# Kernel optimization log

Hardware: AMD Instinct MI355X
Metric: run time of the kernel (lower is better)

## Reference

```python
import jax, jax.numpy as jnp
import numpy as np

B, T, IN, H = 4096, 128, 768, 256


def setup_inputs() -> dict:
    key = jax.random.key(0)
    ks = jax.random.split(key, 5)
    s1 = 1.0 / np.sqrt(IN)
    s2 = 1.0 / np.sqrt(H)
    return {
        "x": jax.random.normal(ks[0], (B, IN), jnp.float32),
        "W1": jax.random.normal(ks[1], (T, IN, H), jnp.float32) * s1,
        "b1": jnp.zeros((T, H), jnp.float32),
        "W2": jax.random.normal(ks[2], (T, H, H), jnp.float32) * s2,
        "b2": jnp.zeros((T, H), jnp.float32),
        "W3": jax.random.normal(ks[3], (T, H), jnp.float32) * s2,
        "b3": jnp.zeros((T,), jnp.float32),
    }


def reference(x, W1, b1, W2, b2, W3, b3):
    # Per-task 3-layer MLP, vectorized over tasks. Dropout is eval-mode (identity).
    h = jax.nn.relu(jnp.einsum('bi,tih->bth', x, W1) + b1)          # [B, T, H]
    h = jax.nn.relu(jnp.einsum('bth,thk->btk', h, W2) + b2)         # [B, T, H]
    out = jnp.einsum('bth,th->bt', h, W3) + b3                      # [B, T]
    return out
```

## Files before the change

### kernel.cpp

```cpp
#include <hip/hip_runtime.h>
#include <cstdint>
#include <cstddef>

#define B_   4096
#define T_   128
#define IN_  768
#define H_   256
#define BM_  128
#define KC1  (IN_ / 32)
#define KC2  (H_ / 32)

typedef __bf16 bf16_t;
typedef bf16_t bf16x8  __attribute__((ext_vector_type(8)));
typedef bf16_t bf16x4  __attribute__((ext_vector_type(4)));
typedef float  floatx16 __attribute__((ext_vector_type(16)));

#define MFMA32(a, b, c) __builtin_amdgcn_mfma_f32_32x32x16_bf16((a), (b), (c), 0, 0, 0)

__device__ __forceinline__ void gl_lds16(const bf16_t* g, bf16_t* l) {
    __builtin_amdgcn_global_load_lds(
        (const __attribute__((address_space(1))) void*)g,
        (__attribute__((address_space(3))) void*)l, 16, 0, 0);
}

__global__ void tile_w_kernel(const float* __restrict__ src, bf16_t* __restrict__ dst,
                              int K, int KC, long long total8) {
    long long o = (long long)blockIdx.x * blockDim.x + threadIdx.x;
    if (o >= total8) return;
    int h  = (int)(o & (H_ - 1));
    long long q = o >> 8;
    int kq = (int)(q & 3);
    int q2 = (int)(q >> 2);
    int kc = q2 % KC;
    int t  = q2 / KC;
    const float* s = src + ((long long)t * K + kc * 32 + kq * 8) * H_ + h;
    bf16x8 v;
#pragma unroll
    for (int e = 0; e < 8; ++e) v[e] = (bf16_t)s[(long long)e * H_];
    *(bf16x8*)(dst + o * 8) = v;
}

__global__ void tile_x_kernel(const float* __restrict__ src, bf16_t* __restrict__ dst,
                              long long total8) {
    long long o = (long long)blockIdx.x * blockDim.x + threadIdx.x;
    if (o >= total8) return;
    int m = (int)(o & (BM_ - 1));
    long long q = o >> 7;
    int kq = (int)(q & 3);
    int q2 = (int)(q >> 2);
    int kc   = q2 % KC1;
    int mblk = q2 / KC1;
    const float* s = src + ((long long)mblk * BM_ + m) * IN_ + kc * 32 + kq * 8;
    float4 a = *(const float4*)s;
    float4 b = *(const float4*)(s + 4);
    bf16x8 v;
    v[0] = (bf16_t)a.x; v[1] = (bf16_t)a.y; v[2] = (bf16_t)a.z; v[3] = (bf16_t)a.w;
    v[4] = (bf16_t)b.x; v[5] = (bf16_t)b.y; v[6] = (bf16_t)b.z; v[7] = (bf16_t)b.w;
    *(bf16x8*)(dst + o * 8) = v;
}

__global__ __launch_bounds__(256, 2)
void mtmlp_fused2(const bf16_t* __restrict__ xt, const bf16_t* __restrict__ w1t,
                  const float* __restrict__ b1, const bf16_t* __restrict__ w2t,
                  const float* __restrict__ b2, const float* __restrict__ W3,
                  const float* __restrict__ b3, float* __restrict__ out) {
    const int mblk = blockIdx.x;
    const int t    = blockIdx.y;
    const int m0   = mblk * BM_;
    const int tid  = threadIdx.x;
    const int lane = tid & 63;
    const int wid  = tid >> 6;
    const int wm   = wid >> 1;
    const int wn   = wid & 1;
    const int ln31 = lane & 31;
    const int hi   = lane >> 5;

    __shared__ __align__(16) bf16_t hbuf[BM_ * H_];
    __shared__ __align__(16) bf16_t wt[4 * H_ * 8];
    bf16_t* xs = hbuf;
    float*  w3s = (float*)wt;

    floatx16 acc[4][2];
#pragma unroll
    for (int i = 0; i < 4; ++i)
#pragma unroll
        for (int j = 0; j < 2; ++j)
#pragma unroll
            for (int e = 0; e < 16; ++e) acc[i][j][e] = 0.0f;

    const bf16_t* w1base = w1t + (size_t)(t * KC1) * 8192;
    const bf16_t* xbase  = xt + (size_t)(mblk * KC1) * 4096;
    for (int kc = 0; kc < KC1; ++kc) {
        __syncthreads();
        {
            const bf16_t* wsrc = w1base + kc * 8192;
            const bf16_t* xsrc = xbase + kc * 4096;
            const int off = wid * 2048 + lane * 8;
#pragma unroll
            for (int r = 0; r < 4; ++r) gl_lds16(wsrc + off + r * 512, wt + off + r * 512);
            const int xoff = wid * 1024 + lane * 8;
#pragma unroll
            for (int r = 0; r < 2; ++r) gl_lds16(xsrc + xoff + r * 512, xs + xoff + r * 512);
        }
        __syncthreads();
#pragma unroll
        for (int s = 0; s < 2; ++s) {
            const int kq = s * 2 + hi;
            bf16x8 A[4], Bf[2];
#pragma unroll
            for (int i = 0; i < 4; ++i)
                A[i] = *(const bf16x8*)(wt + (size_t)(kq * H_ + wm * 128 + i * 32 + ln31) * 8);
#pragma unroll
            for (int j = 0; j < 2; ++j)
                Bf[j] = *(const bf16x8*)(xs + (size_t)(kq * BM_ + wn * 64 + j * 32 + ln31) * 8);
#pragma unroll
            for (int i = 0; i < 4; ++i)
#pragma unroll
                for (int j = 0; j < 2; ++j) acc[i][j] = MFMA32(A[i], Bf[j], acc[i][j]);
        }
    }

    __syncthreads();
#pragma unroll
    for (int i = 0; i < 4; ++i) {
        const int hb = wm * 128 + i * 32;
#pragma unroll
        for (int g = 0; g < 4; ++g) {
            const int h0 = hb + g * 8 + 4 * hi;
            float4 bias = *(const float4*)(b1 + t * H_ + h0);
            const int blk = h0 >> 3;
#pragma unroll
            for (int j = 0; j < 2; ++j) {
                const int m = wn * 64 + j * 32 + ln31;
                bf16x4 o;
                o[0] = (bf16_t)fmaxf(acc[i][j][4 * g + 0] + bias.x, 0.0f);
                o[1] = (bf16_t)fmaxf(acc[i][j][4 * g + 1] + bias.y, 0.0f);
                o[2] = (bf16_t)fmaxf(acc[i][j][4 * g + 2] + bias.z, 0.0f);
                o[3] = (bf16_t)fmaxf(acc[i][j][4 * g + 3] + bias.w, 0.0f);
                *(bf16x4*)(hbuf + (size_t)m * H_ + (blk ^ (m & 7)) * 8 + 4 * hi) = o;
            }
        }
    }

#pragma unroll
    for (int i = 0; i < 4; ++i)
#pragma unroll
        for (int j = 0; j < 2; ++j)
#pragma unroll
            for (int e = 0; e < 16; ++e) acc[i][j][e] = 0.0f;

    const bf16_t* w2base = w2t + (size_t)(t * KC2) * 8192;
    for (int kc = 0; kc < KC2; ++kc) {
        __syncthreads();
        {
            const bf16_t* wsrc = w2base + kc * 8192;
            const int off = wid * 2048 + lane * 8;
#pragma unroll
            for (int r = 0; r < 4; ++r) gl_lds16(wsrc + off + r * 512, wt + off + r * 512);
        }
        __syncthreads();
#pragma unroll
        for (int s = 0; s < 2; ++s) {
            const int kq = s * 2 + hi;
            bf16x8 A[4], Bf[2];
#pragma unroll
            for (int i = 0; i < 4; ++i)
                A[i] = *(const bf16x8*)(wt + (size_t)(kq * H_ + wm * 128 + i * 32 + ln31) * 8);
            const int blk = kc * 4 + kq;
#pragma unroll
            for (int j = 0; j < 2; ++j) {
                const int m = wn * 64 + j * 32 + ln31;
                Bf[j] = *(const bf16x8*)(hbuf + (size_t)m * H_ + (blk ^ (m & 7)) * 8);
            }
#pragma unroll
            for (int i = 0; i < 4; ++i)
#pragma unroll
                for (int j = 0; j < 2; ++j) acc[i][j] = MFMA32(A[i], Bf[j], acc[i][j]);
        }
    }

    __syncthreads();
    w3s[tid] = W3[t * H_ + tid];
#pragma unroll
    for (int i = 0; i < 4; ++i) {
        const int hb = wm * 128 + i * 32;
#pragma unroll
        for (int g = 0; g < 4; ++g) {
            const int h0 = hb + g * 8 + 4 * hi;
            float4 bias = *(const float4*)(b2 + t * H_ + h0);
            const int blk = h0 >> 3;
#pragma unroll
            for (int j = 0; j < 2; ++j) {
                const int m = wn * 64 + j * 32 + ln31;
                bf16x4 o;
                o[0] = (bf16_t)fmaxf(acc[i][j][4 * g + 0] + bias.x, 0.0f);
                o[1] = (bf16_t)fmaxf(acc[i][j][4 * g + 1] + bias.y, 0.0f);
                o[2] = (bf16_t)fmaxf(acc[i][j][4 * g + 2] + bias.z, 0.0f);
                o[3] = (bf16_t)fmaxf(acc[i][j][4 * g + 3] + bias.w, 0.0f);
                *(bf16x4*)(hbuf + (size_t)m * H_ + (blk ^ (m & 7)) * 8 + 4 * hi) = o;
            }
        }
    }
    __syncthreads();

    {
        const int m = tid >> 1, seg = tid & 1;
        float sum = 0.0f;
#pragma unroll
        for (int b = 0; b < 16; ++b) {
            const int blk = seg * 16 + b;
            const bf16x8 v = *(const bf16x8*)(hbuf + (size_t)m * H_ + (blk ^ (m & 7)) * 8);
            const float* w = w3s + blk * 8;
#pragma unroll
            for (int e = 0; e < 8; ++e) sum += (float)v[e] * w[e];
        }
        sum += __shfl_xor(sum, 1);
        if (seg == 0) out[(size_t)(m0 + m) * T_ + t] = sum + b3[t];
    }
}

extern "C" void kernel_launch(void* const* d_in, const int* in_sizes, int n_in,
                              void* d_out, int out_size, void* d_ws, size_t ws_size,
                              hipStream_t stream) {
    const float* x  = (const float*)d_in[0];
    const float* W1 = (const float*)d_in[1];
    const float* b1 = (const float*)d_in[2];
    const float* W2 = (const float*)d_in[3];
    const float* b2 = (const float*)d_in[4];
    const float* W3 = (const float*)d_in[5];
    const float* b3 = (const float*)d_in[6];
    float* out = (float*)d_out;

    const size_t nx  = (size_t)B_ * IN_;
    const size_t nw1 = (size_t)T_ * IN_ * H_;
    const size_t nw2 = (size_t)T_ * H_ * H_;

    bf16_t* xt  = (bf16_t*)d_ws;
    bf16_t* w1t = xt + nx;
    bf16_t* w2t = w1t + nw1;

    tile_x_kernel<<<dim3((unsigned)(nx / 8 / 256)), 256, 0, stream>>>(x, xt, (long long)(nx / 8));
    tile_w_kernel<<<dim3((unsigned)(nw1 / 8 / 256)), 256, 0, stream>>>(W1, w1t, IN_, KC1, (long long)(nw1 / 8));
    tile_w_kernel<<<dim3((unsigned)(nw2 / 8 / 256)), 256, 0, stream>>>(W2, w2t, H_, KC2, (long long)(nw2 / 8));

    dim3 grid(B_ / BM_, T_);
    mtmlp_fused2<<<grid, 256, 0, stream>>>(xt, w1t, b1, w2t, b2, W3, b3, out);
}
```

Measured before the change: 500.6 us.

## Double M tile, double-buffer layer-1 loads, XCD-aware block mapping, vectorized weight tiling

Raises the batch tile per block from 128 to 256 rows with 512 threads, so each weight tile loaded into LDS serves twice as many rows. Layer-1 global-to-LDS loads are double-buffered inside the hidden buffer so staging overlaps MFMA compute. Block indices are remapped so each XCD handles a contiguous set of tasks, which should improve L2 reuse of weights. The hidden buffer drops the XOR swizzle in favour of a k-block-major layout, and the weight tiling kernel now uses float4 reads. The larger LDS footprint and register demand may reduce occupancy, and the unswizzled layout could cause bank conflicts.

New measurement: 474.4 us. -5.2%, faster.

```diff
diff --git a/kernel.cpp b/kernel.cpp
--- a/kernel.cpp
+++ b/kernel.cpp
@@ -6,13 +6,13 @@
 #define T_   128
 #define IN_  768
 #define H_   256
-#define BM_  128
+#define BM_  256
 #define KC1  (IN_ / 32)
 #define KC2  (H_ / 32)
 
 typedef __bf16 bf16_t;
-typedef bf16_t bf16x8  __attribute__((ext_vector_type(8)));
-typedef bf16_t bf16x4  __attribute__((ext_vector_type(4)));
+typedef bf16_t bf16x8 __attribute__((ext_vector_type(8)));
+typedef bf16_t bf16x4 __attribute__((ext_vector_type(4)));
 typedef float  floatx16 __attribute__((ext_vector_type(16)));
 
 #define MFMA32(a, b, c) __builtin_amdgcn_mfma_f32_32x32x16_bf16((a), (b), (c), 0, 0, 0)
@@ -23,34 +23,40 @@
         (__attribute__((address_space(3))) void*)l, 16, 0, 0);
 }
 
-__global__ void tile_w_kernel(const float* __restrict__ src, bf16_t* __restrict__ dst,
-                              int K, int KC, long long total8) {
-    long long o = (long long)blockIdx.x * blockDim.x + threadIdx.x;
-    if (o >= total8) return;
-    int h  = (int)(o & (H_ - 1));
-    long long q = o >> 8;
-    int kq = (int)(q & 3);
-    int q2 = (int)(q >> 2);
-    int kc = q2 % KC;
-    int t  = q2 / KC;
-    const float* s = src + ((long long)t * K + kc * 32 + kq * 8) * H_ + h;
-    bf16x8 v;
-#pragma unroll
-    for (int e = 0; e < 8; ++e) v[e] = (bf16_t)s[(long long)e * H_];
-    *(bf16x8*)(dst + o * 8) = v;
+__global__ __launch_bounds__(256)
+void tile_w2(const float* __restrict__ src, bf16_t* __restrict__ dst, int K, int KC) {
+    const int t  = blockIdx.x / KC;
+    const int kc = blockIdx.x - t * KC;
+    const int kq = threadIdx.x >> 6;
+    const int h4 = (threadIdx.x & 63) * 4;
+    const float* s = src + ((size_t)t * K + kc * 32 + kq * 8) * H_ + h4;
+    float r[8][4];
+#pragma unroll
+    for (int e = 0; e < 8; ++e) {
+        float4 v = *(const float4*)(s + (size_t)e * H_);
+        r[e][0] = v.x; r[e][1] = v.y; r[e][2] = v.z; r[e][3] = v.w;
+    }
+    bf16_t* d = dst + (((size_t)(t * KC + kc) * 4 + kq) * H_ + h4) * 8;
+#pragma unroll
+    for (int c = 0; c < 4; ++c) {
+        bf16x8 v;
+#pragma unroll
+        for (int e = 0; e < 8; ++e) v[e] = (bf16_t)r[e][c];
+        *(bf16x8*)(d + c * 8) = v;
+    }
 }
 
 __global__ void tile_x_kernel(const float* __restrict__ src, bf16_t* __restrict__ dst,
                               long long total8) {
     long long o = (long long)blockIdx.x * blockDim.x + threadIdx.x;
     if (o >= total8) return;
-    int m = (int)(o & (BM_ - 1));
+    int m = (int)(o & 127);
     long long q = o >> 7;
     int kq = (int)(q & 3);
     int q2 = (int)(q >> 2);
     int kc   = q2 % KC1;
     int mblk = q2 / KC1;
-    const float* s = src + ((long long)mblk * BM_ + m) * IN_ + kc * 32 + kq * 8;
+    const float* s = src + ((long long)mblk * 128 + m) * IN_ + kc * 32 + kq * 8;
     float4 a = *(const float4*)s;
     float4 b = *(const float4*)(s + 4);
     bf16x8 v;
@@ -59,26 +65,30 @@
     *(bf16x8*)(dst + o * 8) = v;
 }
 
-__global__ __launch_bounds__(256, 2)
-void mtmlp_fused2(const bf16_t* __restrict__ xt, const bf16_t* __restrict__ w1t,
+__global__ __launch_bounds__(512, 2)
+void mtmlp_fused3(const bf16_t* __restrict__ xt, const bf16_t* __restrict__ w1t,
                   const float* __restrict__ b1, const bf16_t* __restrict__ w2t,
                   const float* __restrict__ b2, const float* __restrict__ W3,
                   const float* __restrict__ b3, float* __restrict__ out) {
-    const int mblk = blockIdx.x;
-    const int t    = blockIdx.y;
+    const int L    = blockIdx.x;
+    const int xcd  = L & 7;
+    const int slot = L >> 3;
+    const int t    = xcd * 16 + (slot >> 4);
+    const int mblk = slot & 15;
     const int m0   = mblk * BM_;
+    const int mb0  = mblk * 2;
+
     const int tid  = threadIdx.x;
     const int lane = tid & 63;
     const int wid  = tid >> 6;
-    const int wm   = wid >> 1;
-    const int wn   = wid & 1;
+    const int wm   = wid >> 2;
+    const int wn   = wid & 3;
     const int ln31 = lane & 31;
     const int hi   = lane >> 5;
 
     __shared__ __align__(16) bf16_t hbuf[BM_ * H_];
-    __shared__ __align__(16) bf16_t wt[4 * H_ * 8];
-    bf16_t* xs = hbuf;
-    float*  w3s = (float*)wt;
+    __shared__ __align__(16) bf16_t wt2[4 * H_ * 8];
+    float* w3s = (float*)wt2;
 
     floatx16 acc[4][2];
 #pragma unroll
@@ -88,56 +98,67 @@
 #pragma unroll
             for (int e = 0; e < 16; ++e) acc[i][j][e] = 0.0f;
 
-    const bf16_t* w1base = w1t + (size_t)(t * KC1) * 8192;
-    const bf16_t* xbase  = xt + (size_t)(mblk * KC1) * 4096;
-    for (int kc = 0; kc < KC1; ++kc) {
-        __syncthreads();
-        {
-            const bf16_t* wsrc = w1base + kc * 8192;
-            const bf16_t* xsrc = xbase + kc * 4096;
-            const int off = wid * 2048 + lane * 8;
-#pragma unroll
-            for (int r = 0; r < 4; ++r) gl_lds16(wsrc + off + r * 512, wt + off + r * 512);
-            const int xoff = wid * 1024 + lane * 8;
-#pragma unroll
-            for (int r = 0; r < 2; ++r) gl_lds16(xsrc + xoff + r * 512, xs + xoff + r * 512);
-        }
-        __syncthreads();
+    const bf16_t* w1base = w1t + (size_t)t * KC1 * 8192;
+    const bf16_t* x0base = xt + (size_t)mb0 * KC1 * 4096;
+    const bf16_t* x1base = xt + (size_t)(mb0 + 1) * KC1 * 4096;
+
+    auto stage1 = [&](bf16_t* buf, int kc) {
+        const bf16_t* ws = w1base + (size_t)kc * 8192;
+        gl_lds16(ws + tid * 8,        buf + tid * 8);
+        gl_lds16(ws + 4096 + tid * 8, buf + 4096 + tid * 8);
+        gl_lds16(x0base + (size_t)kc * 4096 + tid * 8, buf + 8192 + tid * 8);
+        gl_lds16(x1base + (size_t)kc * 4096 + tid * 8, buf + 12288 + tid * 8);
+    };
+    auto comp1 = [&](const bf16_t* buf) {
 #pragma unroll
         for (int s = 0; s < 2; ++s) {
             const int kq = s * 2 + hi;
             bf16x8 A[4], Bf[2];
 #pragma unroll
             for (int i = 0; i < 4; ++i)
-                A[i] = *(const bf16x8*)(wt + (size_t)(kq * H_ + wm * 128 + i * 32 + ln31) * 8);
-#pragma unroll
-            for (int j = 0; j < 2; ++j)
-                Bf[j] = *(const bf16x8*)(xs + (size_t)(kq * BM_ + wn * 64 + j * 32 + ln31) * 8);
+                A[i] = *(const bf16x8*)(buf + (size_t)(kq * H_ + wm * 128 + i * 32 + ln31) * 8);
+#pragma unroll
+            for (int j = 0; j < 2; ++j) {
+                const int mm = wn * 64 + j * 32 + ln31;
+                Bf[j] = *(const bf16x8*)(buf + 8192 + (mm >> 7) * 4096 +
+                                         (size_t)(kq * 128 + (mm & 127)) * 8);
+            }
 #pragma unroll
             for (int i = 0; i < 4; ++i)
 #pragma unroll
                 for (int j = 0; j < 2; ++j) acc[i][j] = MFMA32(A[i], Bf[j], acc[i][j]);
         }
-    }
-
+    };
+
+    bf16_t* buf0 = hbuf;
+    bf16_t* buf1 = hbuf + 16384;
+    stage1(buf0, 0);
+    for (int kc = 0; kc < KC1; kc += 2) {
+        __syncthreads();
+        stage1(buf1, kc + 1);
+        comp1(buf0);
+        __syncthreads();
+        if (kc + 2 < KC1) stage1(buf0, kc + 2);
+        comp1(buf1);
+    }
     __syncthreads();
+
 #pragma unroll
     for (int i = 0; i < 4; ++i) {
-        const int hb = wm * 128 + i * 32;
 #pragma unroll
         for (int g = 0; g < 4; ++g) {
-            const int h0 = hb + g * 8 + 4 * hi;
+            const int h0 = wm * 128 + i * 32 + g * 8 + 4 * hi;
             float4 bias = *(const float4*)(b1 + t * H_ + h0);
             const int blk = h0 >> 3;
 #pragma unroll
             for (int j = 0; j < 2; ++j) {
-                const int m = wn * 64 + j * 32 + ln31;
+                const int mm = wn * 64 + j * 32 + ln31;
                 bf16x4 o;
                 o[0] = (bf16_t)fmaxf(acc[i][j][4 * g + 0] + bias.x, 0.0f);
                 o[1] = (bf16_t)fmaxf(acc[i][j][4 * g + 1] + bias.y, 0.0f);
                 o[2] = (bf16_t)fmaxf(acc[i][j][4 * g + 2] + bias.z, 0.0f);
                 o[3] = (bf16_t)fmaxf(acc[i][j][4 * g + 3] + bias.w, 0.0f);
-                *(bf16x4*)(hbuf + (size_t)m * H_ + (blk ^ (m & 7)) * 8 + 4 * hi) = o;
+                *(bf16x4*)(hbuf + (size_t)(blk * BM_ + mm) * 8 + 4 * hi) = o;
             }
         }
     }
@@ -149,15 +170,12 @@
 #pragma unroll
             for (int e = 0; e < 16; ++e) acc[i][j][e] = 0.0f;
 
-    const bf16_t* w2base = w2t + (size_t)(t * KC2) * 8192;
+    const bf16_t* w2base = w2t + (size_t)t * KC2 * 8192;
     for (int kc = 0; kc < KC2; ++kc) {
         __syncthreads();
-        {
-            const bf16_t* wsrc = w2base + kc * 8192;
-            const int off = wid * 2048 + lane * 8;
-#pragma unroll
-            for (int r = 0; r < 4; ++r) gl_lds16(wsrc + off + r * 512, wt + off + r * 512);
-        }
+        const bf16_t* ws = w2base + (size_t)kc * 8192;
+        gl_lds16(ws + tid * 8,        wt2 + tid * 8);
+        gl_lds16(ws + 4096 + tid * 8, wt2 + 4096 + tid * 8);
         __syncthreads();
 #pragma unroll
         for (int s = 0; s < 2; ++s) {
@@ -165,12 +183,12 @@
             bf16x8 A[4], Bf[2];
 #pragma unroll
             for (int i = 0; i < 4; ++i)
-                A[i] = *(const bf16x8*)(wt + (size_t)(kq * H_ + wm * 128 + i * 32 + ln31) * 8);
+                A[i] = *(const bf16x8*)(wt2 + (size_t)(kq * H_ + wm * 128 + i * 32 + ln31) * 8);
             const int blk = kc * 4 + kq;
 #pragma unroll
             for (int j = 0; j < 2; ++j) {
-                const int m = wn * 64 + j * 32 + ln31;
-                Bf[j] = *(const bf16x8*)(hbuf + (size_t)m * H_ + (blk ^ (m & 7)) * 8);
+                const int mm = wn * 64 + j * 32 + ln31;
+                Bf[j] = *(const bf16x8*)(hbuf + (size_t)(blk * BM_ + mm) * 8);
             }
 #pragma unroll
             for (int i = 0; i < 4; ++i)
@@ -180,24 +198,23 @@
     }
 
     __syncthreads();
-    w3s[tid] = W3[t * H_ + tid];
+    if (tid < H_) w3s[tid] = W3[t * H_ + tid];
 #pragma unroll
     for (int i = 0; i < 4; ++i) {
-        const int hb = wm * 128 + i * 32;
 #pragma unroll
         for (int g = 0; g < 4; ++g) {
-            const int h0 = hb + g * 8 + 4 * hi;
+            const int h0 = wm * 128 + i * 32 + g * 8 + 4 * hi;
             float4 bias = *(const float4*)(b2 + t * H_ + h0);
             const int blk = h0 >> 3;
 #pragma unroll
             for (int j = 0; j < 2; ++j) {
-                const int m = wn * 64 + j * 32 + ln31;
+                const int mm = wn * 64 + j * 32 + ln31;
                 bf16x4 o;
                 o[0] = (bf16_t)fmaxf(acc[i][j][4 * g + 0] + bias.x, 0.0f);
                 o[1] = (bf16_t)fmaxf(acc[i][j][4 * g + 1] + bias.y, 0.0f);
                 o[2] = (bf16_t)fmaxf(acc[i][j][4 * g + 2] + bias.z, 0.0f);
                 o[3] = (bf16_t)fmaxf(acc[i][j][4 * g + 3] + bias.w, 0.0f);
-                *(bf16x4*)(hbuf + (size_t)m * H_ + (blk ^ (m & 7)) * 8 + 4 * hi) = o;
+                *(bf16x4*)(hbuf + (size_t)(blk * BM_ + mm) * 8 + 4 * hi) = o;
             }
         }
     }
@@ -209,7 +226,7 @@
 #pragma unroll
         for (int b = 0; b < 16; ++b) {
             const int blk = seg * 16 + b;
-            const bf16x8 v = *(const bf16x8*)(hbuf + (size_t)m * H_ + (blk ^ (m & 7)) * 8);
+            const bf16x8 v = *(const bf16x8*)(hbuf + (size_t)(blk * BM_ + m) * 8);
             const float* w = w3s + blk * 8;
 #pragma unroll
             for (int e = 0; e < 8; ++e) sum += (float)v[e] * w[e];
@@ -240,9 +257,8 @@
     bf16_t* w2t = w1t + nw1;
 
     tile_x_kernel<<<dim3((unsigned)(nx / 8 / 256)), 256, 0, stream>>>(x, xt, (long long)(nx / 8));
-    tile_w_kernel<<<dim3((unsigned)(nw1 / 8 / 256)), 256, 0, stream>>>(W1, w1t, IN_, KC1, (long long)(nw1 / 8));
-    tile_w_kernel<<<dim3((unsigned)(nw2 / 8 / 256)), 256, 0, stream>>>(W2, w2t, H_, KC2, (long long)(nw2 / 8));
-
-    dim3 grid(B_ / BM_, T_);
-    mtmlp_fused2<<<grid, 256, 0, stream>>>(xt, w1t, b1, w2t, b2, W3, b3, out);
-}
+    tile_w2<<<dim3(T_ * KC1), 256, 0, stream>>>(W1, w1t, IN_, KC1);
+    tile_w2<<<dim3(T_ * KC2), 256, 0, stream>>>(W2, w2t, H_, KC2);
+
+    mtmlp_fused3<<<dim3(2048), 512, 0, stream>>>(xt, w1t, b1, w2t, b2, W3, b3, out);
+}
```
